# Kernel optimization log

Measured on AMD Instinct MI355X. Metric: run time of the kernel, lower is better.

## Reference

```python
import jax, jax.numpy as jnp
import numpy as np

DIM = 128
HOP = 2
NEIGH = [12, 2]  # neighbor_num per hop
ALPHA = 0.2      # leaky-relu slope
NUM_NODE = 50000
B, S = 128, 50
STDV = 1.0 / np.sqrt(DIM)


def _leaky(x):
    return jnp.where(x >= 0, x, ALPHA * x)


def _local_agg(h, adj, a_local):
    # h: [B,S,D], adj: [B,S,S] ints in 0..4, a_local: [4,D]
    a_in = h[:, :, None, :] * h[:, None, :, :]            # [B,S,S,D]
    e = _leaky(jnp.einsum('bijd,kd->kbij', a_in, a_local))  # [4,B,S,S]
    att = jnp.full(adj.shape, -9e15, dtype=h.dtype)
    for k in range(4):
        att = jnp.where(adj == k + 1, e[k], att)
    att = jax.nn.softmax(att, axis=-1)
    return jnp.einsum('bij,bjd->bid', att, h)


def _global_agg(self_v, neigh_v, extra_v, w1, w2, w3, bias):
    # self_v: [B,N,D], neigh_v: [B,N,K,D], extra_v: [B,N,D]
    a = _leaky(jnp.einsum('bnkd,de->bnke', extra_v[:, :, None, :] * neigh_v, w1))
    a = jnp.einsum('bnke,e->bnk', a, w2)
    a = jax.nn.softmax(a, axis=-1)
    agg = jnp.einsum('bnk,bnkd->bnd', a, neigh_v)
    out = jnp.concatenate([self_v, agg], axis=-1) @ w3 + bias
    return jax.nn.relu(out)


def setup_inputs() -> dict:
    key = jax.random.key(0)
    ks = jax.random.split(key, 12)
    u = lambda k, shp: jax.random.uniform(k, shp, jnp.float32, -STDV, STDV)
    return {
        'inputs': jax.random.randint(ks[0], (B, S), 0, NUM_NODE),
        'adj': jax.random.randint(ks[1], (B, S, S), 0, 5),
        'mask_item': jnp.ones((B, S), dtype=jnp.int32),
        'item': jax.random.randint(ks[2], (B, S), 0, NUM_NODE),
        'first_adj': jax.random.randint(ks[3], (B, S * NEIGH[0]), 0, NUM_NODE),
        'adj_all': jax.random.randint(ks[4], (NUM_NODE, 2), 0, NUM_NODE),
        'embedding': u(ks[5], (NUM_NODE, DIM)),
        'a_local': u(ks[6], (4, DIM)),
        'gw1': u(ks[7], (HOP, DIM, DIM)),
        'gw2': u(ks[8], (HOP, DIM)),
        'gw3': u(ks[9], (HOP, 2 * DIM, DIM)),
        'gbias': u(ks[10], (HOP, DIM)),
    }


def reference(inputs, adj, mask_item, item, first_adj, adj_all,
              embedding, a_local, gw1, gw2, gw3, gbias):
    b, s = inputs.shape
    h = embedding[inputs]                                  # [B,S,D]
    h_local = _local_agg(h, adj, a_local)

    m = mask_item.astype(embedding.dtype)[..., None]       # [B,S,1]
    item_emb = embedding[item] * m
    sum_item = jnp.sum(item_emb, 1) / jnp.sum(m, 1)        # [B,D]
    sess = sum_item[:, None, :]                            # [B,1,D]

    # multi-hop neighbor sampling
    neigh1 = first_adj.reshape(b, s * NEIGH[0])            # [B, 600]
    neigh2 = adj_all[neigh1.reshape(-1)].reshape(b, s * NEIGH[0] * NEIGH[1])  # [B,1200]
    ev = [embedding[inputs], embedding[neigh1], embedding[neigh2]]

    for n_hop in range(HOP):
        nxt = []
        for hop in range(HOP - n_hop):
            neigh_v = ev[hop + 1].reshape(b, -1, NEIGH[hop], DIM)
            extra_v = jnp.broadcast_to(sess, (b, ev[hop].shape[1], DIM))
            nxt.append(_global_agg(ev[hop], neigh_v, extra_v,
                                   gw1[n_hop], gw2[n_hop], gw3[n_hop], gbias[n_hop]))
        ev = nxt
    h_global = ev[0].reshape(b, s, DIM)

    # dropout is identity at eval
    return h_local + h_global
```

## Files before the change

### kernel.cpp

```cpp
#include <hip/hip_runtime.h>
#include <stdint.h>

typedef unsigned short ushort_t;
typedef __attribute__((ext_vector_type(8))) short bf16x8;
typedef __attribute__((ext_vector_type(4))) float f32x4;

#define B_   128
#define S_   50
#define D_   128
#define ALPHA_ 0.2f

__device__ __forceinline__ float bf2f(ushort_t u){
  return __uint_as_float(((uint32_t)u) << 16);
}
__device__ __forceinline__ ushort_t f2bf(float f){
  uint32_t x = __float_as_uint(f);
  x = (x + 0x7fffu + ((x >> 16) & 1u)) >> 16;
  return (ushort_t)x;
}
__device__ __forceinline__ float leaky(float x){ return x >= 0.f ? x : ALPHA_*x; }

__device__ __forceinline__ int detect_flag_block(const uint32_t* __restrict__ emb_raw){
  __shared__ int flg;
  if (threadIdx.x == 0){
    int ok = 1;
    for (int i = 0; i < 64; i++){
      uint32_t lo = emb_raw[i] & 0xffffu;
      uint32_t ex = (lo >> 7) & 0xFFu;
      if (!(lo == 0u || (ex >= 64u && ex <= 126u))) ok = 0;
    }
    flg = ok;
  }
  __syncthreads();
  return flg;
}

#define NLOCAL_ 512
#define NSESS_  64
#define NCVT_   6347
#define NPREP_  48

__global__ __launch_bounds__(256) void k1(
    const int* __restrict__ inputs, const int* __restrict__ adj,
    const int* __restrict__ item, const int* __restrict__ mask,
    const void* __restrict__ p0, const void* __restrict__ p1,
    const void* __restrict__ p2, const void* __restrict__ p3,
    const void* __restrict__ p4, const void* __restrict__ p5,
    ushort_t* __restrict__ emb_b, uint4* __restrict__ w1f, uint4* __restrict__ w3f,
    ushort_t* __restrict__ sessb, ushort_t* __restrict__ hlb)
{
  int blk = blockIdx.x, tid = threadIdx.x;
  int flag = detect_flag_block((const uint32_t*)p0);

  if (blk < NLOCAL_){
    __shared__ ushort_t hS[64][136];
    __shared__ float    attS[16][68];
    __shared__ int      sids[64];
    __shared__ ushort_t alS[512];
    int b  = blk >> 2;
    int mi = blk & 3;
    if (tid < 64) sids[tid] = (tid < S_) ? inputs[b*S_ + tid] : 0;
    for (int i = tid; i < 512; i += 256)
      alS[i] = flag ? ((const ushort_t*)p1)[i] : f2bf(((const float*)p1)[i]);
    __syncthreads();
    if (flag){
      const ushort_t* e16 = (const ushort_t*)p0;
      for (int idx = tid; idx < 64*16; idx += 256){
        int j = idx >> 4, ch = idx & 15;
        uint4 v = {0u, 0u, 0u, 0u};
        if (j < S_) v = *(const uint4*)(e16 + (size_t)sids[j]*D_ + ch*8);
        *(uint4*)(&hS[j][ch*8]) = v;
      }
    } else {
      const float* ef = (const float*)p0;
      for (int idx = tid; idx < 64*32; idx += 256){
        int j = idx >> 5, ch = idx & 31;
        union { ushort_t u[4]; uint2 d2; } o;
        o.d2 = make_uint2(0u, 0u);
        if (j < S_){
          float4 v = *(const float4*)(ef + (size_t)sids[j]*D_ + ch*4);
          o.u[0]=f2bf(v.x); o.u[1]=f2bf(v.y); o.u[2]=f2bf(v.z); o.u[3]=f2bf(v.w);
        }
        *(uint2*)(&hS[j][ch*4]) = o.d2;
      }
    }
    for (int idx = tid; idx < 16*64; idx += 256)
      attS[idx >> 6][idx & 63] = -9.0e15f;
    __syncthreads();

    int lane = tid & 63, wv = tid >> 6;
    int q = lane >> 4, c = lane & 15;

    f32x4 Eacc[4];
    #pragma unroll
    for (int ni = 0; ni < 4; ni++) Eacc[ni] = (f32x4){0.f,0.f,0.f,0.f};
    #pragma unroll
    for (int kt = 0; kt < 4; kt++){
      uint4 av = *(const uint4*)(alS + wv*D_ + kt*32 + q*8);
      const uint32_t* ap = (const uint32_t*)&av;
      uint4 hv = *(const uint4*)(&hS[mi*16 + c][kt*32 + q*8]);
      const uint32_t* hp = (const uint32_t*)&hv;
      union { ushort_t u[8]; bf16x8 v; } afr;
      #pragma unroll
      for (int p = 0; p < 4; p++){
        float x0 = __uint_as_float(hp[p] << 16)         * __uint_as_float(ap[p] << 16);
        float x1 = __uint_as_float(hp[p] & 0xffff0000u) * __uint_as_float(ap[p] & 0xffff0000u);
        afr.u[2*p]   = f2bf(x0);
        afr.u[2*p+1] = f2bf(x1);
      }
      #pragma unroll
      for (int ni = 0; ni < 4; ni++){
        union { uint4 q4; bf16x8 v; } bfr;
        bfr.q4 = *(const uint4*)(&hS[ni*16 + c][kt*32 + q*8]);
        Eacc[ni] = __builtin_amdgcn_mfma_f32_16x16x32_bf16(afr.v, bfr.v, Eacc[ni], 0,0,0);
      }
    }
    const int* adjb = adj + (size_t)b*S_*S_;
    #pragma unroll
    for (int ni = 0; ni < 4; ni++){
      int j = ni*16 + c;
      #pragma unroll
      for (int r = 0; r < 4; r++){
        int i = mi*16 + q*4 + r;
        if (i < S_ && j < S_){
          int kk = adjb[i*S_ + j];
          if (kk == wv + 1) attS[q*4 + r][j] = leaky(Eacc[ni][r]);
        }
      }
    }
    __syncthreads();
    {
      int r  = tid >> 4;
      int cg = tid & 15;
      int i  = mi*16 + r;
      float v0 = attS[r][cg*4+0], v1 = attS[r][cg*4+1];
      float v2 = attS[r][cg*4+2], v3 = attS[r][cg*4+3];
      float mx = fmaxf(fmaxf(v0,v1), fmaxf(v2,v3));
      #pragma unroll
      for (int off = 1; off < 16; off <<= 1) mx = fmaxf(mx, __shfl_xor(mx, off, 16));
      float e0 = (cg*4+0 < S_) ? __expf(v0 - mx) : 0.f;
      float e1 = (cg*4+1 < S_) ? __expf(v1 - mx) : 0.f;
      float e2 = (cg*4+2 < S_) ? __expf(v2 - mx) : 0.f;
      float e3 = (cg*4+3 < S_) ? __expf(v3 - mx) : 0.f;
      float s = e0 + e1 + e2 + e3;
      #pragma unroll
      for (int off = 1; off < 16; off <<= 1) s += __shfl_xor(s, off, 16);
      float inv = (i < S_) ? 1.f / s : 0.f;
      attS[r][cg*4+0] = e0*inv;
      attS[r][cg*4+1] = e1*inv;
      attS[r][cg*4+2] = e2*inv;
      attS[r][cg*4+3] = e3*inv;
    }
    __syncthreads();
    f32x4 Pacc[2];
    Pacc[0] = (f32x4){0.f,0.f,0.f,0.f};
    Pacc[1] = (f32x4){0.f,0.f,0.f,0.f};
    #pragma unroll
    for (int kt = 0; kt < 2; kt++){
      union { ushort_t u[8]; bf16x8 v; } afr;
      const float* arow = &attS[c][kt*32 + q*8];
      #pragma unroll
      for (int j = 0; j < 8; j++) afr.u[j] = f2bf(arow[j]);
      #pragma unroll
      for (int nn = 0; nn < 2; nn++){
        int ni = 2*wv + nn;
        union { ushort_t u[8]; bf16x8 v; } bfr;
        #pragma unroll
        for (int jj = 0; jj < 8; jj++)
          bfr.u[jj] = hS[kt*32 + q*8 + jj][ni*16 + c];
        Pacc[nn] = __builtin_amdgcn_mfma_f32_16x16x32_bf16(afr.v, bfr.v, Pacc[nn], 0,0,0);
      }
    }
    #pragma unroll
    for (int nn = 0; nn < 2; nn++){
      int d = (2*wv + nn)*16 + c;
      #pragma unroll
      for (int r = 0; r < 4; r++){
        int i = mi*16 + q*4 + r;
        if (i < S_) hlb[((size_t)b*S_ + i)*D_ + d] = f2bf(Pacc[nn][r]);
      }
    }
  } else if (blk < NLOCAL_ + NSESS_){
    int b = (blk - NLOCAL_)*2 + (tid >> 7);
    int d = tid & 127;
    float acc = 0.f, den = 0.f;
    if (flag){
      const ushort_t* e16 = (const ushort_t*)p0;
      for (int s = 0; s < S_; s++){
        float fm = (float)mask[b*S_ + s];
        int id = item[b*S_ + s];
        acc += fm * bf2f(e16[(size_t)id*D_ + d]);
        den += fm;
      }
    } else {
      const float* ef = (const float*)p0;
      for (int s = 0; s < S_; s++){
        float fm = (float)mask[b*S_ + s];
        int id = item[b*S_ + s];
        acc += fm * ef[(size_t)id*D_ + d];
        den += fm;
      }
    }
    sessb[b*D_ + d] = f2bf(acc / den);
  } else if (blk < NLOCAL_ + NSESS_ + NCVT_){
    const int seg_end[6] = {6400000, 6400512, 6433280, 6433536, 6499072, 6499328};
    int base = ((blk - NLOCAL_ - NSESS_)*256 + tid) * 4;
    if (base >= 6499328) return;
    int s = 0;
    while (base >= seg_end[s]) s++;
    int segbase = (s == 0) ? 0 : seg_end[s-1];
    const void* src = (s==0)?p0:(s==1)?p1:(s==2)?p2:(s==3)?p3:(s==4)?p4:p5;
    int off = base - segbase;
    union { ushort_t u[4]; uint2 d2; } o;
    if (flag){
      o.d2 = *(const uint2*)((const ushort_t*)src + off);
    } else {
      float4 v = *(const float4*)((const float*)src + off);
      o.u[0] = f2bf(v.x); o.u[1] = f2bf(v.y); o.u[2] = f2bf(v.z); o.u[3] = f2bf(v.w);
    }
    *(uint2*)(emb_b + base) = o.d2;
  } else {
    int id = (blk - NLOCAL_ - NSESS_ - NCVT_)*256 + tid;
    if (id >= 12288) return;
    if (id < 4096){
      int h = id >> 11, i = id & 2047;
      int kt = i >> 9, rem = i & 511, t = rem >> 6, ln = rem & 63;
      int q = ln >> 4, c = ln & 15;
      union { ushort_t u[8]; uint4 q4; } e;
      #pragma unroll
      for (int j = 0; j < 8; j++){
        int idx = h*16384 + (32*kt + q*8 + j)*128 + 16*t + c;
        e.u[j] = flag ? ((const ushort_t*)p2)[idx] : f2bf(((const float*)p2)[idx]);
      }
      w1f[h*2048 + i] = e.q4;
    } else {
      int id2 = id - 4096;
      int h = id2 >> 12, i = id2 & 4095;
      int kt = i >> 9, rem = i & 511, t = rem >> 6, ln = rem & 63;
      int q = ln >> 4, c = ln & 15;
      union { ushort_t u[8]; uint4 q4; } e;
      #pragma unroll
      for (int j = 0; j < 8; j++){
        int idx = h*32768 + (32*kt + q*8 + j)*128 + 16*t + c;
        e.u[j] = flag ? ((const ushort_t*)p4)[idx] : f2bf(((const float*)p4)[idx]);
      }
      w3f[h*4096 + i] = e.q4;
    }
  }
}

__global__ __launch_bounds__(512) void tprep(
    const ushort_t* __restrict__ emb, const uint4* __restrict__ w3f,
    ushort_t* __restrict__ Tt, ushort_t* __restrict__ Tb)
{
  __shared__ uint4 frag[4096];
  int tid = threadIdx.x;
  for (int i = tid; i < 4096; i += 512) frag[i] = w3f[i];
  __syncthreads();
  int lane = tid & 63, wave = tid >> 6;
  int m = lane & 15, q = lane >> 4;
  int row = blockIdx.x*128 + wave*16 + m;
  int rowc = row < 50000 ? row : 49999;
  f32x4 acct[8], accb[8];
  #pragma unroll
  for (int t = 0; t < 8; t++){ acct[t] = (f32x4){0.f,0.f,0.f,0.f}; accb[t] = (f32x4){0.f,0.f,0.f,0.f}; }
  #pragma unroll
  for (int kt = 0; kt < 4; kt++){
    union { uint4 q4; bf16x8 v; } bfr;
    bfr.q4 = *(const uint4*)(emb + (size_t)rowc*D_ + kt*32 + q*8);
    #pragma unroll
    for (int t = 0; t < 8; t++){
      union { uint4 q4; bf16x8 v; } af, af2;
      af.q4  = frag[(kt*8 + t)*64 + lane];
      af2.q4 = frag[((kt+4)*8 + t)*64 + lane];
      acct[t] = __builtin_amdgcn_mfma_f32_16x16x32_bf16(af.v,  bfr.v, acct[t], 0, 0, 0);
      accb[t] = __builtin_amdgcn_mfma_f32_16x16x32_bf16(af2.v, bfr.v, accb[t], 0, 0, 0);
    }
  }
  if (row < 50000){
    #pragma unroll
    for (int t = 0; t < 8; t++){
      int col0 = 16*t + q*4;
      union { ushort_t u[4]; uint2 d2; } pk;
      #pragma unroll
      for (int r = 0; r < 4; r++) pk.u[r] = f2bf(acct[t][r]);
      *(uint2*)(Tt + (size_t)row*D_ + col0) = pk.d2;
      #pragma unroll
      for (int r = 0; r < 4; r++) pk.u[r] = f2bf(accb[t][r]);
      *(uint2*)(Tb + (size_t)row*D_ + col0) = pk.d2;
    }
  }
}

__global__ __launch_bounds__(256) void score_mfma_ab(
    const ushort_t* __restrict__ sessb, const ushort_t* __restrict__ emb,
    const int* __restrict__ neigh1, const int* __restrict__ adj_all,
    const uint4* __restrict__ w1f, const ushort_t* __restrict__ w2,
    float* __restrict__ score, int nA){
  __shared__ uint4 bfrag[2048];
  int tid = threadIdx.x;
  for (int i = tid; i < 2048; i += 256) bfrag[i] = w1f[i];
  __syncthreads();
  int lane = tid & 63, wave = tid >> 6;
  int m = lane & 15, q = lane >> 4;
  float w2v[8];
  #pragma unroll
  for (int t = 0; t < 8; t++) w2v[t] = bf2f(w2[16*t + m]);

  for (int it = 0; it < 2; it++){
    int row_base = blockIdx.x*128 + it*64 + wave*16;
    int row = row_base + m;
    const ushort_t* nrow; int b;
    if (row < nA){
      nrow = emb + (size_t)neigh1[row]*D_;
      b = row / 600;
    } else {
      int r2 = row - nA;
      nrow = emb + (size_t)adj_all[(size_t)neigh1[r2>>1]*2 + (r2&1)]*D_;
      b = r2 / 1200;
    }
    const ushort_t* srow = sessb + (size_t)b*D_;

    f32x4 acc[8];
    #pragma unroll
    for (int t = 0; t < 8; t++) acc[t] = (f32x4){0.f,0.f,0.f,0.f};
    #pragma unroll
    for (int kt = 0; kt < 4; kt++){
      uint4 nv = *(const uint4*)(nrow + kt*32 + q*8);
      uint4 sv = *(const uint4*)(srow + kt*32 + q*8);
      const uint32_t* np = (const uint32_t*)&nv;
      const uint32_t* sp = (const uint32_t*)&sv;
      union { ushort_t u[8]; bf16x8 v; } afr;
      #pragma unroll
      for (int p = 0; p < 4; p++){
        uint32_t n2 = np[p], s2 = sp[p];
        float a0 = __uint_as_float(n2 << 16)          * __uint_as_float(s2 << 16);
        float a1 = __uint_as_float(n2 & 0xffff0000u)  * __uint_as_float(s2 & 0xffff0000u);
        afr.u[2*p]   = f2bf(a0);
        afr.u[2*p+1] = f2bf(a1);
      }
      #pragma unroll
      for (int t = 0; t < 8; t++){
        union { uint4 q4; bf16x8 v; } bfr;
        bfr.q4 = bfrag[(kt*8 + t)*64 + lane];
        acc[t] = __builtin_amdgcn_mfma_f32_16x16x32_bf16(afr.v, bfr.v, acc[t], 0, 0, 0);
      }
    }
    #pragma unroll
    for (int r = 0; r < 4; r++){
      float s = 0.f;
      #pragma unroll
      for (int t = 0; t < 8; t++) s += leaky(acc[t][r]) * w2v[t];
      s += __shfl_xor(s, 1, 64);
      s += __shfl_xor(s, 2, 64);
      s += __shfl_xor(s, 4, 64);
      s += __shfl_xor(s, 8, 64);
      if (m == 0) score[row_base + q*4 + r] = s;
    }
  }
}

__global__ __launch_bounds__(256) void score_mfma_c(
    const ushort_t* __restrict__ sessb, const ushort_t* __restrict__ out1,
    const uint4* __restrict__ w1f, const ushort_t* __restrict__ w2,
    float* __restrict__ score){
  __shared__ uint4 bfrag[2048];
  int tid = threadIdx.x;
  for (int i = tid; i < 2048; i += 256) bfrag[i] = w1f[i];
  __syncthreads();
  int lane = tid & 63, wave = tid >> 6;
  int m = lane & 15, q = lane >> 4;
  float w2v[8];
  #pragma unroll
  for (int t = 0; t < 8; t++) w2v[t] = bf2f(w2[16*t + m]);
  for (int it = 0; it < 2; it++){
    int row_base = blockIdx.x*128 + it*64 + wave*16;
    int row = row_base + m;
    const ushort_t* nrow = out1 + (size_t)row*D_;
    int b = row / 600;
    const ushort_t* srow = sessb + (size_t)b*D_;
    f32x4 acc[8];
    #pragma unroll
    for (int t = 0; t < 8; t++) acc[t] = (f32x4){0.f,0.f,0.f,0.f};
    #pragma unroll
    for (int kt = 0; kt < 4; kt++){
      uint4 nv = *(const uint4*)(nrow + kt*32 + q*8);
      uint4 sv = *(const uint4*)(srow + kt*32 + q*8);
      const uint32_t* np = (const uint32_t*)&nv;
      const uint32_t* sp = (const uint32_t*)&sv;
      union { ushort_t u[8]; bf16x8 v; } afr;
      #pragma unroll
      for (int p = 0; p < 4; p++){
        uint32_t n2 = np[p], s2 = sp[p];
        float a0 = __uint_as_float(n2 << 16)          * __uint_as_float(s2 << 16);
        float a1 = __uint_as_float(n2 & 0xffff0000u)  * __uint_as_float(s2 & 0xffff0000u);
        afr.u[2*p]   = f2bf(a0);
        afr.u[2*p+1] = f2bf(a1);
      }
      #pragma unroll
      for (int t = 0; t < 8; t++){
        union { uint4 q4; bf16x8 v; } bfr;
        bfr.q4 = bfrag[(kt*8 + t)*64 + lane];
        acc[t] = __builtin_amdgcn_mfma_f32_16x16x32_bf16(afr.v, bfr.v, acc[t], 0, 0, 0);
      }
    }
    #pragma unroll
    for (int r = 0; r < 4; r++){
      float s = 0.f;
      #pragma unroll
      for (int t = 0; t < 8; t++) s += leaky(acc[t][r]) * w2v[t];
      s += __shfl_xor(s, 1, 64);
      s += __shfl_xor(s, 2, 64);
      s += __shfl_xor(s, 4, 64);
      s += __shfl_xor(s, 8, 64);
      if (m == 0) score[row_base + q*4 + r] = s;
    }
  }
}

template<int K>
__device__ __forceinline__ void softmaxK(const float* __restrict__ sc, float att[K]){
  float mx = -__builtin_inff();
  #pragma unroll
  for (int k = 0; k < K; k++){ att[k] = sc[k]; mx = fmaxf(mx, att[k]); }
  float s = 0.f;
  #pragma unroll
  for (int k = 0; k < K; k++){ att[k] = __expf(att[k] - mx); s += att[k]; }
  float inv = 1.f / s;
  #pragma unroll
  for (int k = 0; k < K; k++) att[k] *= inv;
}

template<int K>
__device__ __forceinline__ void out_tile(
    int lane, const uint4* __restrict__ afrag,
    const ushort_t* __restrict__ sptr, const ushort_t* const nptr[K],
    const float att[K], f32x4 acc[8]){
  int q = lane >> 4;
  #pragma unroll
  for (int kt = 0; kt < 8; kt++){
    union { ushort_t u[8]; uint4 q4; bf16x8 v; } bfr;
    if (kt < 4){
      bfr.q4 = *(const uint4*)(sptr + kt*32 + q*8);
    } else {
      float g[8] = {0,0,0,0,0,0,0,0};
      #pragma unroll
      for (int k = 0; k < K; k++){
        uint4 nv = *(const uint4*)(nptr[k] + (kt-4)*32 + q*8);
        const uint32_t* np = (const uint32_t*)&nv;
        #pragma unroll
        for (int p = 0; p < 4; p++){
          g[2*p]   = fmaf(att[k], __uint_as_float(np[p] << 16),         g[2*p]);
          g[2*p+1] = fmaf(att[k], __uint_as_float(np[p] & 0xffff0000u), g[2*p+1]);
        }
      }
      #pragma unroll
      for (int j = 0; j < 8; j++) bfr.u[j] = f2bf(g[j]);
    }
    #pragma unroll
    for (int t = 0; t < 8; t++){
      union { uint4 q4; bf16x8 v; } af;
      af.q4 = afrag[(kt*8 + t)*64 + lane];
      acc[t] = __builtin_amdgcn_mfma_f32_16x16x32_bf16(af.v, bfr.v, acc[t], 0, 0, 0);
    }
  }
}

__global__ __launch_bounds__(256) void gather_out(
    const int* __restrict__ idx, const int* __restrict__ nbr,
    const int* __restrict__ adj_all, const float* __restrict__ score,
    const ushort_t* __restrict__ Tt, const ushort_t* __restrict__ Tb,
    const ushort_t* __restrict__ bias,
    ushort_t* __restrict__ o0c, ushort_t* __restrict__ out1c,
    int nA50, int nTot, int scoreBbase)
{
  int row  = (blockIdx.x*256 + threadIdx.x) >> 6;
  int lane = threadIdx.x & 63;
  if (row >= nTot) return;
  row = __builtin_amdgcn_readfirstlane(row);
  float b0 = bf2f(bias[lane*2]), b1 = bf2f(bias[lane*2 + 1]);
  float acc0, acc1;
  ushort_t* dst;
  if (row < nA50){
    float att[12];
    softmaxK<12>(score + (size_t)row*12, att);
    uint32_t sv = *(const uint32_t*)(Tt + (size_t)idx[row]*D_ + lane*2);
    acc0 = __uint_as_float(sv << 16);
    acc1 = __uint_as_float(sv & 0xffff0000u);
    #pragma unroll
    for (int k = 0; k < 12; k++){
      uint32_t nv = *(const uint32_t*)(Tb + (size_t)nbr[row*12 + k]*D_ + lane*2);
      acc0 = fmaf(att[k], __uint_as_float(nv << 16),          acc0);
      acc1 = fmaf(att[k], __uint_as_float(nv & 0xffff0000u),  acc1);
    }
    dst = o0c + (size_t)row*D_;
  } else {
    int rB = row - nA50;
    float att[2];
    softmaxK<2>(score + scoreBbase + (size_t)rB*2, att);
    int self = nbr[rB];
    uint32_t sv = *(const uint32_t*)(Tt + (size_t)self*D_ + lane*2);
    acc0 = __uint_as_float(sv << 16);
    acc1 = __uint_as_float(sv & 0xffff0000u);
    #pragma unroll
    for (int k = 0; k < 2; k++){
      uint32_t nv = *(const uint32_t*)(Tb + (size_t)adj_all[(size_t)self*2 + k]*D_ + lane*2);
      acc0 = fmaf(att[k], __uint_as_float(nv << 16),          acc0);
      acc1 = fmaf(att[k], __uint_as_float(nv & 0xffff0000u),  acc1);
    }
    dst = out1c + (size_t)rB*D_;
  }
  union { ushort_t u[2]; uint32_t d; } pk;
  pk.u[0] = f2bf(fmaxf(acc0 + b0, 0.f));
  pk.u[1] = f2bf(fmaxf(acc1 + b1, 0.f));
  *(uint32_t*)(dst + lane*2) = pk.d;
}

__global__ __launch_bounds__(512) void out_mfma_ab(
    const float* __restrict__ score, const int* __restrict__ idx,
    const int* __restrict__ nbr, const int* __restrict__ adj_all,
    const ushort_t* __restrict__ emb, const uint4* __restrict__ w3f,
    const ushort_t* __restrict__ bias,
    ushort_t* __restrict__ o0c, ushort_t* __restrict__ out1c,
    int nA, int nTot, int scoreBbase){
  __shared__ uint4 afrag[4096];
  int tid = threadIdx.x;
  for (int i = tid; i < 4096; i += 512) afrag[i] = w3f[i];
  __syncthreads();
  int lane = tid & 63, wave = tid >> 6;
  int mrow = lane & 15, q = lane >> 4;
  float bv[8][4];
  #pragma unroll
  for (int t = 0; t < 8; t++){
    const ushort_t* bp = bias + 16*t + q*4;
    #pragma unroll
    for (int r = 0; r < 4; r++) bv[t][r] = bf2f(bp[r]);
  }
  int row_base = blockIdx.x*128 + wave*16;
  int row = row_base + mrow;
  bool active = row < nTot;
  int rowc = active ? row : (nTot - 1);
  bool isA = rowc < nA;
  f32x4 acc[8];
  #pragma unroll
  for (int t = 0; t < 8; t++) acc[t] = (f32x4){0.f,0.f,0.f,0.f};
  if (isA){
    const ushort_t* sptr = emb + (size_t)idx[rowc]*D_;
    const ushort_t* nptr[12];
    #pragma unroll
    for (int k = 0; k < 12; k++) nptr[k] = emb + (size_t)nbr[rowc*12 + k]*D_;
    float att[12];
    softmaxK<12>(score + (size_t)rowc*12, att);
    out_tile<12>(lane, afrag, sptr, nptr, att, acc);
  } else {
    int rB = rowc - nA;
    const ushort_t* sptr = emb + (size_t)nbr[rB]*D_;
    const ushort_t* nptr[2];
    #pragma unroll
    for (int k = 0; k < 2; k++) nptr[k] = emb + (size_t)adj_all[(size_t)nbr[rB]*2 + k]*D_;
    float att[2];
    softmaxK<2>(score + scoreBbase + (size_t)rB*2, att);
    out_tile<2>(lane, afrag, sptr, nptr, att, acc);
  }
  if (active){
    ushort_t* dst = isA ? (o0c + (size_t)row*D_) : (out1c + (size_t)(row - nA)*D_);
    #pragma unroll
    for (int t = 0; t < 8; t++){
      int col0 = 16*t + q*4;
      union { ushort_t u[4]; uint2 d2; } pk;
      #pragma unroll
// ... 26 lines not shown
  bool active = row < nrows;
  int rowc = active ? row : (nrows - 1);
  const ushort_t* sptr = selfsrc + (size_t)rowc*D_;
  const ushort_t* nptr[12];
  #pragma unroll
  for (int k = 0; k < 12; k++) nptr[k] = out1 + (size_t)(rowc*12 + k)*D_;
  float att[12];
  softmaxK<12>(score + (size_t)rowc*12, att);
  f32x4 acc[8];
  #pragma unroll
  for (int t = 0; t < 8; t++) acc[t] = (f32x4){0.f,0.f,0.f,0.f};
  out_tile<12>(lane, afrag, sptr, nptr, att, acc);
  if (active){
    #pragma unroll
    for (int t = 0; t < 8; t++){
      int col0 = 16*t + q*4;
      float v[4];
      const ushort_t* ap = addsrc + (size_t)row*D_ + col0;
      #pragma unroll
      for (int r = 0; r < 4; r++)
        v[r] = fmaxf(acc[t][r] + bv[t][r], 0.f) + bf2f(ap[r]);
      *(f32x4*)(outf + (size_t)row*D_ + col0) = (f32x4){v[0], v[1], v[2], v[3]};
    }
  }
}

extern "C" void kernel_launch(void* const* d_in, const int* in_sizes, int n_in,
                              void* d_out, int out_size, void* d_ws, size_t ws_size,
                              hipStream_t stream) {
  const int* inputs    = (const int*)d_in[0];
  const int* adj       = (const int*)d_in[1];
  const int* mask_item = (const int*)d_in[2];
  const int* item      = (const int*)d_in[3];
  const int* first_adj = (const int*)d_in[4];
  const int* adj_all   = (const int*)d_in[5];

  char* ws = (char*)d_ws;
  size_t o = 0;
  ushort_t* emb_b  = (ushort_t*)(ws + o); o += 12800000;
  ushort_t* alocb  = (ushort_t*)(ws + o); o += 1024;
  ushort_t* gw1b   = (ushort_t*)(ws + o); o += 65536;
  ushort_t* gw2b   = (ushort_t*)(ws + o); o += 512;
  ushort_t* gw3b   = (ushort_t*)(ws + o); o += 131072;
  ushort_t* gbb    = (ushort_t*)(ws + o); o += 512;
  ushort_t* sessb  = (ushort_t*)(ws + o); o += 32768;
  ushort_t* hlb    = (ushort_t*)(ws + o); o += 1638400;
  uint4*    w1f    = (uint4*)(ws + o);    o += 65536;
  uint4*    w3f    = (uint4*)(ws + o);    o += 131072;
  size_t fixed = o;
  (void)alocb; (void)gw1b; (void)gw3b;

  float* outp = (float*)d_out;

  k1<<<NLOCAL_ + NSESS_ + NCVT_ + NPREP_, 256, 0, stream>>>(
      inputs, adj, item, mask_item,
      d_in[6], d_in[7], d_in[8], d_in[9], d_in[10], d_in[11],
      emb_b, w1f, w3f, sessb, hlb);

  const size_t TPATH_NEED = fixed + 2*(size_t)12800000
                          + (size_t)128*153600
                          + (size_t)128*12800
                          + (size_t)3*128*600*4;
  if (ws_size >= TPATH_NEED){
    ushort_t* Tt    = (ushort_t*)(ws + o);  o += 12800000;
    ushort_t* Tb    = (ushort_t*)(ws + o);  o += 12800000;
    ushort_t* out1c = (ushort_t*)(ws + o);  o += (size_t)128*153600;
    ushort_t* o0c   = (ushort_t*)(ws + o);  o += (size_t)128*12800;
    float*    score = (float*)(ws + o);
    int nA600 = 128*600, nA50 = 128*50, nTot = 128*650;

    tprep<<<391, 512, 0, stream>>>(emb_b, w3f, Tt, Tb);
    score_mfma_ab<<<(3*nA600)/128, 256, 0, stream>>>(sessb, emb_b, first_adj, adj_all,
                                                     w1f, gw2b, score, nA600);
    gather_out<<<(nTot*64 + 255)/256, 256, 0, stream>>>(inputs, first_adj, adj_all, score,
                                                        Tt, Tb, gbb, o0c, out1c,
                                                        nA50, nTot, nA600);
    score_mfma_c<<<nA600/128, 256, 0, stream>>>(sessb, out1c, w1f + 2048, gw2b + 128, score);
    out_mfma_c<<<(nA50 + 127)/128, 512, 0, stream>>>(score, out1c, o0c,
                                                     w3f + 4096, gbb + 128,
                                                     hlb, outp, nA50);
  } else {
    int CHB = 16;
    if      (ws_size >= fixed + (size_t)128*173600) CHB = 128;
    else if (ws_size >= fixed + (size_t)64 *173600) CHB = 64;
    else if (ws_size >= fixed + (size_t)32 *173600) CHB = 32;
    ushort_t* out1c = (ushort_t*)(ws + o);  o += (size_t)CHB*153600;
    ushort_t* o0c   = (ushort_t*)(ws + o);  o += (size_t)CHB*12800;
    float*    score = (float*)(ws + o);

    int nchunk = B_ / CHB;
    for (int c = 0; c < nchunk; c++){
      int b0 = c * CHB;
      const int* fadj  = first_adj + (size_t)b0 * 600;
      const ushort_t* sbc = sessb + (size_t)b0 * D_;
      ushort_t*  hlc   = hlb  + (size_t)b0 * 50 * D_;
      float*     outc  = outp + (size_t)b0 * 50 * D_;
      int nA600 = CHB*600, nA50 = CHB*50, nTot = CHB*650;

      score_mfma_ab<<<(3*nA600)/128, 256, 0, stream>>>(sbc, emb_b, fadj, adj_all,
                                                       w1f, gw2b, score, nA600);
      out_mfma_ab<<<(nTot + 127)/128, 512, 0, stream>>>(score, inputs + b0*50, fadj, adj_all,
                                                        emb_b, w3f, gbb, o0c, out1c,
                                                        nA50, nTot, nA600);
      score_mfma_c<<<nA600/128, 256, 0, stream>>>(sbc, out1c, w1f + 2048, gw2b + 128, score);
      out_mfma_c<<<(nA50 + 127)/128, 512, 0, stream>>>(score, out1c, o0c,
                                                       w3f + 4096, gbb + 128,
                                                       hlc, outc, nA50);
    }
  }
}
```

Measured before the change: 194.0 us.

## Fuse transform precompute into k1 and fold session vector into per-batch W1

Moves the embedding-times-W3 precompute (Tt/Tb) from its own kernel into extra blocks of the first fused kernel, converting directly from the raw input embeddings. The score kernels are restructured per batch: the session vector is multiplied into the W1 fragments once per block, so neighbor rows feed the MFMA directly with no elementwise product. Grid shapes change to per-batch row groups, and the final output kernel uses smaller 64-row blocks for more parallelism. The cost is W1 fragments rebuilt per block and more shared-memory sharing inside k1, which could lower occupancy for the local-attention blocks.

```diff
diff --git a/kernel.cpp b/kernel.cpp
--- a/kernel.cpp
+++ b/kernel.cpp
@@ -37,8 +37,13 @@
 
 #define NLOCAL_ 512
 #define NSESS_  64
+#define NTPREP_ 1564
 #define NCVT_   6347
 #define NPREP_  48
+#define TPREP_BASE_ (NLOCAL_ + NSESS_)
+#define CVT_BASE_   (TPREP_BASE_ + NTPREP_)
+#define PREP_BASE_  (CVT_BASE_ + NCVT_)
+#define K1_GRID_    (PREP_BASE_ + NPREP_)
 
 __global__ __launch_bounds__(256) void k1(
     const int* __restrict__ inputs, const int* __restrict__ adj,
@@ -47,29 +52,31 @@
     const void* __restrict__ p2, const void* __restrict__ p3,
     const void* __restrict__ p4, const void* __restrict__ p5,
     ushort_t* __restrict__ emb_b, uint4* __restrict__ w1f, uint4* __restrict__ w3f,
-    ushort_t* __restrict__ sessb, ushort_t* __restrict__ hlb)
+    ushort_t* __restrict__ sessb, ushort_t* __restrict__ hlb,
+    ushort_t* __restrict__ Tt, ushort_t* __restrict__ Tb)
 {
+  __shared__ uint4 smem[2048];
   int blk = blockIdx.x, tid = threadIdx.x;
   int flag = detect_flag_block((const uint32_t*)p0);
 
   if (blk < NLOCAL_){
-    __shared__ ushort_t hS[64][136];
-    __shared__ float    attS[16][68];
-    __shared__ int      sids[64];
-    __shared__ ushort_t alS[512];
+    ushort_t* hSp   = (ushort_t*)smem;
+    float*    attSp = (float*)((char*)smem + 17408);
+    int*      sidsp = (int*)((char*)smem + 21760);
+    ushort_t* alSp  = (ushort_t*)((char*)smem + 22016);
     int b  = blk >> 2;
     int mi = blk & 3;
-    if (tid < 64) sids[tid] = (tid < S_) ? inputs[b*S_ + tid] : 0;
+    if (tid < 64) sidsp[tid] = (tid < S_) ? inputs[b*S_ + tid] : 0;
     for (int i = tid; i < 512; i += 256)
-      alS[i] = flag ? ((const ushort_t*)p1)[i] : f2bf(((const float*)p1)[i]);
+      alSp[i] = flag ? ((const ushort_t*)p1)[i] : f2bf(((const float*)p1)[i]);
     __syncthreads();
     if (flag){
       const ushort_t* e16 = (const ushort_t*)p0;
       for (int idx = tid; idx < 64*16; idx += 256){
         int j = idx >> 4, ch = idx & 15;
         uint4 v = {0u, 0u, 0u, 0u};
-        if (j < S_) v = *(const uint4*)(e16 + (size_t)sids[j]*D_ + ch*8);
-        *(uint4*)(&hS[j][ch*8]) = v;
+        if (j < S_) v = *(const uint4*)(e16 + (size_t)sidsp[j]*D_ + ch*8);
+        *(uint4*)(hSp + j*136 + ch*8) = v;
       }
     } else {
       const float* ef = (const float*)p0;
@@ -78,14 +85,14 @@
         union { ushort_t u[4]; uint2 d2; } o;
         o.d2 = make_uint2(0u, 0u);
         if (j < S_){
-          float4 v = *(const float4*)(ef + (size_t)sids[j]*D_ + ch*4);
+          float4 v = *(const float4*)(ef + (size_t)sidsp[j]*D_ + ch*4);
           o.u[0]=f2bf(v.x); o.u[1]=f2bf(v.y); o.u[2]=f2bf(v.z); o.u[3]=f2bf(v.w);
         }
-        *(uint2*)(&hS[j][ch*4]) = o.d2;
+        *(uint2*)(hSp + j*136 + ch*4) = o.d2;
       }
     }
     for (int idx = tid; idx < 16*64; idx += 256)
-      attS[idx >> 6][idx & 63] = -9.0e15f;
+      attSp[(idx >> 6)*68 + (idx & 63)] = -9.0e15f;
     __syncthreads();
 
     int lane = tid & 63, wv = tid >> 6;
@@ -96,9 +103,9 @@
     for (int ni = 0; ni < 4; ni++) Eacc[ni] = (f32x4){0.f,0.f,0.f,0.f};
     #pragma unroll
     for (int kt = 0; kt < 4; kt++){
-      uint4 av = *(const uint4*)(alS + wv*D_ + kt*32 + q*8);
+      uint4 av = *(const uint4*)(alSp + wv*D_ + kt*32 + q*8);
       const uint32_t* ap = (const uint32_t*)&av;
-      uint4 hv = *(const uint4*)(&hS[mi*16 + c][kt*32 + q*8]);
+      uint4 hv = *(const uint4*)(hSp + (mi*16 + c)*136 + kt*32 + q*8);
       const uint32_t* hp = (const uint32_t*)&hv;
       union { ushort_t u[8]; bf16x8 v; } afr;
       #pragma unroll
@@ -111,7 +118,7 @@
       #pragma unroll
       for (int ni = 0; ni < 4; ni++){
         union { uint4 q4; bf16x8 v; } bfr;
-        bfr.q4 = *(const uint4*)(&hS[ni*16 + c][kt*32 + q*8]);
+        bfr.q4 = *(const uint4*)(hSp + (ni*16 + c)*136 + kt*32 + q*8);
         Eacc[ni] = __builtin_amdgcn_mfma_f32_16x16x32_bf16(afr.v, bfr.v, Eacc[ni], 0,0,0);
       }
     }
@@ -124,7 +131,7 @@
         int i = mi*16 + q*4 + r;
         if (i < S_ && j < S_){
           int kk = adjb[i*S_ + j];
-          if (kk == wv + 1) attS[q*4 + r][j] = leaky(Eacc[ni][r]);
+          if (kk == wv + 1) attSp[(q*4 + r)*68 + j] = leaky(Eacc[ni][r]);
         }
       }
     }
@@ -133,8 +140,8 @@
       int r  = tid >> 4;
       int cg = tid & 15;
       int i  = mi*16 + r;
-      float v0 = attS[r][cg*4+0], v1 = attS[r][cg*4+1];
-      float v2 = attS[r][cg*4+2], v3 = attS[r][cg*4+3];
+      float v0 = attSp[r*68 + cg*4+0], v1 = attSp[r*68 + cg*4+1];
+      float v2 = attSp[r*68 + cg*4+2], v3 = attSp[r*68 + cg*4+3];
       float mx = fmaxf(fmaxf(v0,v1), fmaxf(v2,v3));
       #pragma unroll
       for (int off = 1; off < 16; off <<= 1) mx = fmaxf(mx, __shfl_xor(mx, off, 16));
@@ -146,10 +153,10 @@
       #pragma unroll
       for (int off = 1; off < 16; off <<= 1) s += __shfl_xor(s, off, 16);
       float inv = (i < S_) ? 1.f / s : 0.f;
-      attS[r][cg*4+0] = e0*inv;
-      attS[r][cg*4+1] = e1*inv;
-      attS[r][cg*4+2] = e2*inv;
-      attS[r][cg*4+3] = e3*inv;
+      attSp[r*68 + cg*4+0] = e0*inv;
+      attSp[r*68 + cg*4+1] = e1*inv;
+      attSp[r*68 + cg*4+2] = e2*inv;
+      attSp[r*68 + cg*4+3] = e3*inv;
     }
     __syncthreads();
     f32x4 Pacc[2];
@@ -158,7 +165,7 @@
     #pragma unroll
     for (int kt = 0; kt < 2; kt++){
       union { ushort_t u[8]; bf16x8 v; } afr;
-      const float* arow = &attS[c][kt*32 + q*8];
+      const float* arow = attSp + c*68 + kt*32 + q*8;
       #pragma unroll
       for (int j = 0; j < 8; j++) afr.u[j] = f2bf(arow[j]);
       #pragma unroll
@@ -167,7 +174,7 @@
         union { ushort_t u[8]; bf16x8 v; } bfr;
         #pragma unroll
         for (int jj = 0; jj < 8; jj++)
-          bfr.u[jj] = hS[kt*32 + q*8 + jj][ni*16 + c];
+          bfr.u[jj] = hSp[(kt*32 + q*8 + jj)*136 + ni*16 + c];
         Pacc[nn] = __builtin_amdgcn_mfma_f32_16x16x32_bf16(afr.v, bfr.v, Pacc[nn], 0,0,0);
       }
     }
@@ -202,9 +209,63 @@
       }
     }
     sessb[b*D_ + d] = f2bf(acc / den);
-  } else if (blk < NLOCAL_ + NSESS_ + NCVT_){
+  } else if (blk < CVT_BASE_){
+    if (!Tt) return;
+    int tp   = blk - TPREP_BASE_;
+    int half = tp & 1;
+    int rowbase = (tp >> 1) * 64;
+    for (int i = tid; i < 2048; i += 256){
+      int kt = i >> 9, rem = i & 511, t = rem >> 6, ln = rem & 63;
+      int q = ln >> 4, c = ln & 15;
+      union { ushort_t u[8]; uint4 q4; } e;
+      #pragma unroll
+      for (int j = 0; j < 8; j++){
+        int idx = (32*(half*4 + kt) + q*8 + j)*128 + 16*t + c;
+        e.u[j] = flag ? ((const ushort_t*)p4)[idx] : f2bf(((const float*)p4)[idx]);
+      }
+      smem[i] = e.q4;
+    }
+    __syncthreads();
+    int lane = tid & 63, wave = tid >> 6;
+    int m = lane & 15, q = lane >> 4;
+    int row = rowbase + wave*16 + m;
+    int rowc = row < 50000 ? row : 49999;
+    f32x4 acc[8];
+    #pragma unroll
+    for (int t = 0; t < 8; t++) acc[t] = (f32x4){0.f,0.f,0.f,0.f};
+    #pragma unroll
+    for (int kt = 0; kt < 4; kt++){
+      union { ushort_t u[8]; uint4 q4; bf16x8 v; } bfr;
+      if (flag){
+        bfr.q4 = *(const uint4*)((const ushort_t*)p0 + (size_t)rowc*D_ + kt*32 + q*8);
+      } else {
+        const float* ef = (const float*)p0 + (size_t)rowc*D_ + kt*32 + q*8;
+        float4 f0 = *(const float4*)(ef);
+        float4 f1 = *(const float4*)(ef + 4);
+        bfr.u[0]=f2bf(f0.x); bfr.u[1]=f2bf(f0.y); bfr.u[2]=f2bf(f0.z); bfr.u[3]=f2bf(f0.w);
+        bfr.u[4]=f2bf(f1.x); bfr.u[5]=f2bf(f1.y); bfr.u[6]=f2bf(f1.z); bfr.u[7]=f2bf(f1.w);
+      }
+      #pragma unroll
+      for (int t = 0; t < 8; t++){
+        union { uint4 q4; bf16x8 v; } af;
+        af.q4 = smem[(kt*8 + t)*64 + lane];
+        acc[t] = __builtin_amdgcn_mfma_f32_16x16x32_bf16(af.v, bfr.v, acc[t], 0, 0, 0);
+      }
+    }
+    if (row < 50000){
+      ushort_t* dst = (half ? Tb : Tt) + (size_t)row*D_;
+      #pragma unroll
+      for (int t = 0; t < 8; t++){
+        int col0 = 16*t + q*4;
+        union { ushort_t u[4]; uint2 d2; } pk;
+        #pragma unroll
+        for (int r = 0; r < 4; r++) pk.u[r] = f2bf(acc[t][r]);
+        *(uint2*)(dst + col0) = pk.d2;
+      }
+    }
+  } else if (blk < PREP_BASE_){
     const int seg_end[6] = {6400000, 6400512, 6433280, 6433536, 6499072, 6499328};
-    int base = ((blk - NLOCAL_ - NSESS_)*256 + tid) * 4;
+    int base = ((blk - CVT_BASE_)*256 + tid) * 4;
     if (base >= 6499328) return;
     int s = 0;
     while (base >= seg_end[s]) s++;
@@ -220,7 +281,7 @@
     }
     *(uint2*)(emb_b + base) = o.d2;
   } else {
-    int id = (blk - NLOCAL_ - NSESS_ - NCVT_)*256 + tid;
+    int id = (blk - PREP_BASE_)*256 + tid;
     if (id >= 12288) return;
     if (id < 4096){
       int h = id >> 11, i = id & 2047;
@@ -249,57 +310,32 @@
   }
 }
 
-__global__ __launch_bounds__(512) void tprep(
-    const ushort_t* __restrict__ emb, const uint4* __restrict__ w3f,
-    ushort_t* __restrict__ Tt, ushort_t* __restrict__ Tb)
-{
-  __shared__ uint4 frag[4096];
-  int tid = threadIdx.x;
-  for (int i = tid; i < 4096; i += 512) frag[i] = w3f[i];
-  __syncthreads();
-  int lane = tid & 63, wave = tid >> 6;
-  int m = lane & 15, q = lane >> 4;
-  int row = blockIdx.x*128 + wave*16 + m;
-  int rowc = row < 50000 ? row : 49999;
-  f32x4 acct[8], accb[8];
-  #pragma unroll
-  for (int t = 0; t < 8; t++){ acct[t] = (f32x4){0.f,0.f,0.f,0.f}; accb[t] = (f32x4){0.f,0.f,0.f,0.f}; }
-  #pragma unroll
-  for (int kt = 0; kt < 4; kt++){
-    union { uint4 q4; bf16x8 v; } bfr;
-    bfr.q4 = *(const uint4*)(emb + (size_t)rowc*D_ + kt*32 + q*8);
-    #pragma unroll
-    for (int t = 0; t < 8; t++){
-      union { uint4 q4; bf16x8 v; } af, af2;
-      af.q4  = frag[(kt*8 + t)*64 + lane];
-      af2.q4 = frag[((kt+4)*8 + t)*64 + lane];
-      acct[t] = __builtin_amdgcn_mfma_f32_16x16x32_bf16(af.v,  bfr.v, acct[t], 0, 0, 0);
-      accb[t] = __builtin_amdgcn_mfma_f32_16x16x32_bf16(af2.v, bfr.v, accb[t], 0, 0, 0);
-    }
-  }
-  if (row < 50000){
-    #pragma unroll
-    for (int t = 0; t < 8; t++){
-      int col0 = 16*t + q*4;
-      union { ushort_t u[4]; uint2 d2; } pk;
-      #pragma unroll
-      for (int r = 0; r < 4; r++) pk.u[r] = f2bf(acct[t][r]);
-      *(uint2*)(Tt + (size_t)row*D_ + col0) = pk.d2;
-      #pragma unroll
-      for (int r = 0; r < 4; r++) pk.u[r] = f2bf(accb[t][r]);
-      *(uint2*)(Tb + (size_t)row*D_ + col0) = pk.d2;
-    }
-  }
-}
-
-__global__ __launch_bounds__(256) void score_mfma_ab(
+__global__ __launch_bounds__(256) void score2_ab(
     const ushort_t* __restrict__ sessb, const ushort_t* __restrict__ emb,
     const int* __restrict__ neigh1, const int* __restrict__ adj_all,
     const uint4* __restrict__ w1f, const ushort_t* __restrict__ w2,
-    float* __restrict__ score, int nA){
+    float* __restrict__ score)
+{
   __shared__ uint4 bfrag[2048];
-  int tid = threadIdx.x;
-  for (int i = tid; i < 2048; i += 256) bfrag[i] = w1f[i];
+  __shared__ ushort_t sS[128];
+  int blk = blockIdx.x, tid = threadIdx.x;
+  int sb  = blk / 6;
+  int sub = blk - sb*6;
+  int grp = sub >> 1;
+  int halft = sub & 1;
+  if (tid < 16) ((uint4*)sS)[tid] = ((const uint4*)(sessb + (size_t)sb*D_))[tid];
+  __syncthreads();
+  for (int i = tid; i < 2048; i += 256){
+    int kt = i >> 9, ln = i & 63, q = (ln >> 4);
+    uint4 w = w1f[i];
+    uint4 sv = *(const uint4*)(sS + kt*32 + q*8);
+    const ushort_t* wu = (const ushort_t*)&w;
+    const ushort_t* su = (const ushort_t*)&sv;
+    union { ushort_t u[8]; uint4 q4; } o;
+    #pragma unroll
+    for (int j = 0; j < 8; j++) o.u[j] = f2bf(bf2f(wu[j]) * bf2f(su[j]));
+    bfrag[i] = o.q4;
+  }
   __syncthreads();
   int lane = tid & 63, wave = tid >> 6;
   int m = lane & 15, q = lane >> 4;
@@ -307,113 +343,115 @@
   #pragma unroll
   for (int t = 0; t < 8; t++) w2v[t] = bf2f(w2[16*t + m]);
 
-  for (int it = 0; it < 2; it++){
-    int row_base = blockIdx.x*128 + it*64 + wave*16;
-    int row = row_base + m;
-    const ushort_t* nrow; int b;
-    if (row < nA){
-      nrow = emb + (size_t)neigh1[row]*D_;
-      b = row / 600;
+  int tend = halft ? 38 : 19;
+  for (int t = halft*19 + wave; t < tend; t += 4){
+    int rr = t*16 + m;
+    int rrc = rr < 599 ? rr : 599;
+    int nid;
+    if (grp == 0){
+      nid = neigh1[sb*600 + rrc];
     } else {
-      int r2 = row - nA;
-      nrow = emb + (size_t)adj_all[(size_t)neigh1[r2>>1]*2 + (r2&1)]*D_;
-      b = r2 / 1200;
-    }
-    const ushort_t* srow = sessb + (size_t)b*D_;
-
+      int r2 = sb*1200 + (grp-1)*600 + rrc;
+      nid = adj_all[(size_t)neigh1[r2 >> 1]*2 + (r2 & 1)];
+    }
+    const ushort_t* nrow = emb + (size_t)nid*D_;
     f32x4 acc[8];
     #pragma unroll
-    for (int t = 0; t < 8; t++) acc[t] = (f32x4){0.f,0.f,0.f,0.f};
+    for (int t8 = 0; t8 < 8; t8++) acc[t8] = (f32x4){0.f,0.f,0.f,0.f};
     #pragma unroll
     for (int kt = 0; kt < 4; kt++){
-      uint4 nv = *(const uint4*)(nrow + kt*32 + q*8);
-      uint4 sv = *(const uint4*)(srow + kt*32 + q*8);
-      const uint32_t* np = (const uint32_t*)&nv;
-      const uint32_t* sp = (const uint32_t*)&sv;
-      union { ushort_t u[8]; bf16x8 v; } afr;
-      #pragma unroll
-      for (int p = 0; p < 4; p++){
-        uint32_t n2 = np[p], s2 = sp[p];
-        float a0 = __uint_as_float(n2 << 16)          * __uint_as_float(s2 << 16);
-        float a1 = __uint_as_float(n2 & 0xffff0000u)  * __uint_as_float(s2 & 0xffff0000u);
-        afr.u[2*p]   = f2bf(a0);
-        afr.u[2*p+1] = f2bf(a1);
-      }
-      #pragma unroll
-      for (int t = 0; t < 8; t++){
-        union { uint4 q4; bf16x8 v; } bfr;
-        bfr.q4 = bfrag[(kt*8 + t)*64 + lane];
-        acc[t] = __builtin_amdgcn_mfma_f32_16x16x32_bf16(afr.v, bfr.v, acc[t], 0, 0, 0);
+      union { uint4 q4; bf16x8 v; } af;
+      af.q4 = *(const uint4*)(nrow + kt*32 + q*8);
+      #pragma unroll
+      for (int t8 = 0; t8 < 8; t8++){
+        union { uint4 q4; bf16x8 v; } bf;
+        bf.q4 = bfrag[(kt*8 + t8)*64 + lane];
+        acc[t8] = __builtin_amdgcn_mfma_f32_16x16x32_bf16(af.v, bf.v, acc[t8], 0, 0, 0);
       }
     }
     #pragma unroll
     for (int r = 0; r < 4; r++){
       float s = 0.f;
       #pragma unroll
-      for (int t = 0; t < 8; t++) s += leaky(acc[t][r]) * w2v[t];
+      for (int t8 = 0; t8 < 8; t8++) s += leaky(acc[t8][r]) * w2v[t8];
       s += __shfl_xor(s, 1, 64);
       s += __shfl_xor(s, 2, 64);
       s += __shfl_xor(s, 4, 64);
       s += __shfl_xor(s, 8, 64);
-      if (m == 0) score[row_base + q*4 + r] = s;
-    }
-  }
-}
-
-__global__ __launch_bounds__(256) void score_mfma_c(
+      if (m == 0){
+        int rw = t*16 + q*4 + r;
+        if (rw < 600){
+          int sidx = (grp == 0) ? (sb*600 + rw)
+                                : (76800 + sb*1200 + (grp-1)*600 + rw);
+          score[sidx] = s;
+        }
+      }
+    }
+  }
+}
+
+__global__ __launch_bounds__(256) void score2_c(
     const ushort_t* __restrict__ sessb, const ushort_t* __restrict__ out1,
     const uint4* __restrict__ w1f, const ushort_t* __restrict__ w2,
-    float* __restrict__ score){
+    float* __restrict__ score)
+{
   __shared__ uint4 bfrag[2048];
-  int tid = threadIdx.x;
-  for (int i = tid; i < 2048; i += 256) bfrag[i] = w1f[i];
+  __shared__ ushort_t sS[128];
+  int blk = blockIdx.x, tid = threadIdx.x;
+  int sb  = blk >> 2;
+  int qtr = blk & 3;
+  if (tid < 16) ((uint4*)sS)[tid] = ((const uint4*)(sessb + (size_t)sb*D_))[tid];
+  __syncthreads();
+  for (int i = tid; i < 2048; i += 256){
+    int kt = i >> 9, ln = i & 63, q = (ln >> 4);
+    uint4 w = w1f[i];
+    uint4 sv = *(const uint4*)(sS + kt*32 + q*8);
+    const ushort_t* wu = (const ushort_t*)&w;
+    const ushort_t* su = (const ushort_t*)&sv;
+    union { ushort_t u[8]; uint4 q4; } o;
+    #pragma unroll
+    for (int j = 0; j < 8; j++) o.u[j] = f2bf(bf2f(wu[j]) * bf2f(su[j]));
+    bfrag[i] = o.q4;
+  }
   __syncthreads();
   int lane = tid & 63, wave = tid >> 6;
   int m = lane & 15, q = lane >> 4;
   float w2v[8];
   #pragma unroll
   for (int t = 0; t < 8; t++) w2v[t] = bf2f(w2[16*t + m]);
-  for (int it = 0; it < 2; it++){
-    int row_base = blockIdx.x*128 + it*64 + wave*16;
-    int row = row_base + m;
-    const ushort_t* nrow = out1 + (size_t)row*D_;
-    int b = row / 600;
-    const ushort_t* srow = sessb + (size_t)b*D_;
+
+  int t0 = qtr*10, tend = (qtr*10 + 10 < 38) ? qtr*10 + 10 : 38;
+  for (int t = t0 + wave; t < tend; t += 4){
+    int rr = t*16 + m;
+    int rrc = rr < 599 ? rr : 599;
+    const ushort_t* nrow = out1 + ((size_t)sb*600 + rrc)*D_;
     f32x4 acc[8];
     #pragma unroll
-    for (int t = 0; t < 8; t++) acc[t] = (f32x4){0.f,0.f,0.f,0.f};
+    for (int t8 = 0; t8 < 8; t8++) acc[t8] = (f32x4){0.f,0.f,0.f,0.f};
     #pragma unroll
     for (int kt = 0; kt < 4; kt++){
-      uint4 nv = *(const uint4*)(nrow + kt*32 + q*8);
-      uint4 sv = *(const uint4*)(srow + kt*32 + q*8);
-      const uint32_t* np = (const uint32_t*)&nv;
-      const uint32_t* sp = (const uint32_t*)&sv;
-      union { ushort_t u[8]; bf16x8 v; } afr;
-      #pragma unroll
-      for (int p = 0; p < 4; p++){
-        uint32_t n2 = np[p], s2 = sp[p];
-        float a0 = __uint_as_float(n2 << 16)          * __uint_as_float(s2 << 16);
-        float a1 = __uint_as_float(n2 & 0xffff0000u)  * __uint_as_float(s2 & 0xffff0000u);
-        afr.u[2*p]   = f2bf(a0);
-        afr.u[2*p+1] = f2bf(a1);
-      }
-      #pragma unroll
-      for (int t = 0; t < 8; t++){
-        union { uint4 q4; bf16x8 v; } bfr;
-        bfr.q4 = bfrag[(kt*8 + t)*64 + lane];
-        acc[t] = __builtin_amdgcn_mfma_f32_16x16x32_bf16(afr.v, bfr.v, acc[t], 0, 0, 0);
+      union { uint4 q4; bf16x8 v; } af;
+      af.q4 = *(const uint4*)(nrow + kt*32 + q*8);
+      #pragma unroll
+      for (int t8 = 0; t8 < 8; t8++){
+        union { uint4 q4; bf16x8 v; } bf;
+        bf.q4 = bfrag[(kt*8 + t8)*64 + lane];
+        acc[t8] = __builtin_amdgcn_mfma_f32_16x16x32_bf16(af.v, bf.v, acc[t8], 0, 0, 0);
       }
     }
     #pragma unroll
     for (int r = 0; r < 4; r++){
       float s = 0.f;
       #pragma unroll
-      for (int t = 0; t < 8; t++) s += leaky(acc[t][r]) * w2v[t];
+      for (int t8 = 0; t8 < 8; t8++) s += leaky(acc[t8][r]) * w2v[t8];
       s += __shfl_xor(s, 1, 64);
       s += __shfl_xor(s, 2, 64);
       s += __shfl_xor(s, 4, 64);
       s += __shfl_xor(s, 8, 64);
-      if (m == 0) score[row_base + q*4 + r] = s;
+      if (m == 0){
+        int rw = t*16 + q*4 + r;
+        if (rw < 600) score[sb*600 + rw] = s;
+      }
     }
   }
 }
@@ -516,6 +554,178 @@
   *(uint32_t*)(dst + lane*2) = pk.d;
 }
 
+__global__ __launch_bounds__(256) void out_mfma_c2(
+    const float* __restrict__ score, const ushort_t* __restrict__ out1,
+    const ushort_t* __restrict__ selfsrc, const uint4* __restrict__ w3f,
+    const ushort_t* __restrict__ bias,
+    const ushort_t* __restrict__ addsrc, float* __restrict__ outf, int nrows){
+  __shared__ uint4 afrag[4096];
+  int tid = threadIdx.x;
+  for (int i = tid; i < 4096; i += 256) afrag[i] = w3f[i];
+  __syncthreads();
+  int lane = tid & 63, wave = tid >> 6;
+  int mrow = lane & 15, q = lane >> 4;
+  float bv[8][4];
+  #pragma unroll
+  for (int t = 0; t < 8; t++){
+    const ushort_t* bp = bias + 16*t + q*4;
+    #pragma unroll
+    for (int r = 0; r < 4; r++) bv[t][r] = bf2f(bp[r]);
+  }
+  int row_base = blockIdx.x*64 + wave*16;
+  int row = row_base + mrow;
+  bool active = row < nrows;
+  int rowc = active ? row : (nrows - 1);
+  const ushort_t* sptr = selfsrc + (size_t)rowc*D_;
+  const ushort_t* nptr[12];
+  #pragma unroll
+  for (int k = 0; k < 12; k++) nptr[k] = out1 + (size_t)(rowc*12 + k)*D_;
+  float att[12];
+  softmaxK<12>(score + (size_t)rowc*12, att);
+  f32x4 acc[8];
+  #pragma unroll
+  for (int t = 0; t < 8; t++) acc[t] = (f32x4){0.f,0.f,0.f,0.f};
+  out_tile<12>(lane, afrag, sptr, nptr, att, acc);
+  if (active){
+    #pragma unroll
+    for (int t = 0; t < 8; t++){
+      int col0 = 16*t + q*4;
+      float v[4];
+      const ushort_t* ap = addsrc + (size_t)row*D_ + col0;
+      #pragma unroll
+      for (int r = 0; r < 4; r++)
+        v[r] = fmaxf(acc[t][r] + bv[t][r], 0.f) + bf2f(ap[r]);
+      *(f32x4*)(outf + (size_t)row*D_ + col0) = (f32x4){v[0], v[1], v[2], v[3]};
+    }
+  }
+}
+
+__global__ __launch_bounds__(256) void score_mfma_ab(
+    const ushort_t* __restrict__ sessb, const ushort_t* __restrict__ emb,
+    const int* __restrict__ neigh1, const int* __restrict__ adj_all,
+    const uint4* __restrict__ w1f, const ushort_t* __restrict__ w2,
+    float* __restrict__ score, int nA){
+  __shared__ uint4 bfrag[2048];
+  int tid = threadIdx.x;
+  for (int i = tid; i < 2048; i += 256) bfrag[i] = w1f[i];
+  __syncthreads();
+  int lane = tid & 63, wave = tid >> 6;
+  int m = lane & 15, q = lane >> 4;
+  float w2v[8];
+  #pragma unroll
+  for (int t = 0; t < 8; t++) w2v[t] = bf2f(w2[16*t + m]);
+
+  for (int it = 0; it < 2; it++){
+    int row_base = blockIdx.x*128 + it*64 + wave*16;
+    int row = row_base + m;
+    const ushort_t* nrow; int b;
+    if (row < nA){
+      nrow = emb + (size_t)neigh1[row]*D_;
+      b = row / 600;
+    } else {
+      int r2 = row - nA;
+      nrow = emb + (size_t)adj_all[(size_t)neigh1[r2>>1]*2 + (r2&1)]*D_;
+      b = r2 / 1200;
+    }
+    const ushort_t* srow = sessb + (size_t)b*D_;
+
+    f32x4 acc[8];
+    #pragma unroll
+    for (int t = 0; t < 8; t++) acc[t] = (f32x4){0.f,0.f,0.f,0.f};
+    #pragma unroll
+    for (int kt = 0; kt < 4; kt++){
+      uint4 nv = *(const uint4*)(nrow + kt*32 + q*8);
+      uint4 sv = *(const uint4*)(srow + kt*32 + q*8);
+      const uint32_t* np = (const uint32_t*)&nv;
+      const uint32_t* sp = (const uint32_t*)&sv;
+      union { ushort_t u[8]; bf16x8 v; } afr;
+      #pragma unroll
+      for (int p = 0; p < 4; p++){
+        uint32_t n2 = np[p], s2 = sp[p];
+        float a0 = __uint_as_float(n2 << 16)          * __uint_as_float(s2 << 16);
+        float a1 = __uint_as_float(n2 & 0xffff0000u)  * __uint_as_float(s2 & 0xffff0000u);
+        afr.u[2*p]   = f2bf(a0);
+        afr.u[2*p+1] = f2bf(a1);
+      }
+      #pragma unroll
+      for (int t = 0; t < 8; t++){
+        union { uint4 q4; bf16x8 v; } bfr;
+        bfr.q4 = bfrag[(kt*8 + t)*64 + lane];
+        acc[t] = __builtin_amdgcn_mfma_f32_16x16x32_bf16(afr.v, bfr.v, acc[t], 0, 0, 0);
+      }
+    }
+    #pragma unroll
+    for (int r = 0; r < 4; r++){
+      float s = 0.f;
+      #pragma unroll
+      for (int t = 0; t < 8; t++) s += leaky(acc[t][r]) * w2v[t];
+      s += __shfl_xor(s, 1, 64);
+      s += __shfl_xor(s, 2, 64);
+      s += __shfl_xor(s, 4, 64);
+      s += __shfl_xor(s, 8, 64);
+      if (m == 0) score[row_base + q*4 + r] = s;
+    }
+  }
+}
+
+__global__ __launch_bounds__(256) void score_mfma_c(
+    const ushort_t* __restrict__ sessb, const ushort_t* __restrict__ out1,
+    const uint4* __restrict__ w1f, const ushort_t* __restrict__ w2,
+    float* __restrict__ score){
+  __shared__ uint4 bfrag[2048];
+  int tid = threadIdx.x;
+  for (int i = tid; i < 2048; i += 256) bfrag[i] = w1f[i];
+  __syncthreads();
+  int lane = tid & 63, wave = tid >> 6;
+  int m = lane & 15, q = lane >> 4;
+  float w2v[8];
+  #pragma unroll
+  for (int t = 0; t < 8; t++) w2v[t] = bf2f(w2[16*t + m]);
+  for (int it = 0; it < 2; it++){
+    int row_base = blockIdx.x*128 + it*64 + wave*16;
+    int row = row_base + m;
+    const ushort_t* nrow = out1 + (size_t)row*D_;
+    int b = row / 600;
+    const ushort_t* srow = sessb + (size_t)b*D_;
+    f32x4 acc[8];
+    #pragma unroll
+    for (int t = 0; t < 8; t++) acc[t] = (f32x4){0.f,0.f,0.f,0.f};
+    #pragma unroll
+    for (int kt = 0; kt < 4; kt++){
+      uint4 nv = *(const uint4*)(nrow + kt*32 + q*8);
+      uint4 sv = *(const uint4*)(srow + kt*32 + q*8);
+      const uint32_t* np = (const uint32_t*)&nv;
+      const uint32_t* sp = (const uint32_t*)&sv;
+      union { ushort_t u[8]; bf16x8 v; } afr;
+      #pragma unroll
+      for (int p = 0; p < 4; p++){
+        uint32_t n2 = np[p], s2 = sp[p];
+        float a0 = __uint_as_float(n2 << 16)          * __uint_as_float(s2 << 16);
+        float a1 = __uint_as_float(n2 & 0xffff0000u)  * __uint_as_float(s2 & 0xffff0000u);
+        afr.u[2*p]   = f2bf(a0);
+        afr.u[2*p+1] = f2bf(a1);
+      }
+      #pragma unroll
+      for (int t = 0; t < 8; t++){
+        union { uint4 q4; bf16x8 v; } bfr;
+        bfr.q4 = bfrag[(kt*8 + t)*64 + lane];
+        acc[t] = __builtin_amdgcn_mfma_f32_16x16x32_bf16(afr.v, bfr.v, acc[t], 0, 0, 0);
+      }
+    }
+    #pragma unroll
+    for (int r = 0; r < 4; r++){
+      float s = 0.f;
+      #pragma unroll
+      for (int t = 0; t < 8; t++) s += leaky(acc[t][r]) * w2v[t];
+      s += __shfl_xor(s, 1, 64);
+      s += __shfl_xor(s, 2, 64);
+      s += __shfl_xor(s, 4, 64);
+      s += __shfl_xor(s, 8, 64);
+      if (m == 0) score[row_base + q*4 + r] = s;
+    }
+  }
+}
+
 __global__ __launch_bounds__(512) void out_mfma_ab(
     const float* __restrict__ score, const int* __restrict__ idx,
     const int* __restrict__ nbr, const int* __restrict__ adj_all,
@@ -648,33 +858,38 @@
 
   float* outp = (float*)d_out;
 
-  k1<<<NLOCAL_ + NSESS_ + NCVT_ + NPREP_, 256, 0, stream>>>(
-      inputs, adj, item, mask_item,
-      d_in[6], d_in[7], d_in[8], d_in[9], d_in[10], d_in[11],
-      emb_b, w1f, w3f, sessb, hlb);
-
   const size_t TPATH_NEED = fixed + 2*(size_t)12800000
                           + (size_t)128*153600
                           + (size_t)128*12800
                           + (size_t)3*128*600*4;
-  if (ws_size >= TPATH_NEED){
-    ushort_t* Tt    = (ushort_t*)(ws + o);  o += 12800000;
-    ushort_t* Tb    = (ushort_t*)(ws + o);  o += 12800000;
+  bool tpath = (ws_size >= TPATH_NEED);
+
+  ushort_t* Tt = nullptr; ushort_t* Tb = nullptr;
+  if (tpath){
+    Tt = (ushort_t*)(ws + o);  o += 12800000;
+    Tb = (ushort_t*)(ws + o);  o += 12800000;
+  }
+
+  k1<<<K1_GRID_, 256, 0, stream>>>(
+      inputs, adj, item, mask_item,
+      d_in[6], d_in[7], d_in[8], d_in[9], d_in[10], d_in[11],
+      emb_b, w1f, w3f, sessb, hlb, Tt, Tb);
+
+  if (tpath){
     ushort_t* out1c = (ushort_t*)(ws + o);  o += (size_t)128*153600;
     ushort_t* o0c   = (ushort_t*)(ws + o);  o += (size_t)128*12800;
     float*    score = (float*)(ws + o);
     int nA600 = 128*600, nA50 = 128*50, nTot = 128*650;
 
-    tprep<<<391, 512, 0, stream>>>(emb_b, w3f, Tt, Tb);
-    score_mfma_ab<<<(3*nA600)/128, 256, 0, stream>>>(sessb, emb_b, first_adj, adj_all,
-                                                     w1f, gw2b, score, nA600);
+    score2_ab<<<768, 256, 0, stream>>>(sessb, emb_b, first_adj, adj_all,
+                                       w1f, gw2b, score);
     gather_out<<<(nTot*64 + 255)/256, 256, 0, stream>>>(inputs, first_adj, adj_all, score,
                                                         Tt, Tb, gbb, o0c, out1c,
                                                         nA50, nTot, nA600);
-    score_mfma_c<<<nA600/128, 256, 0, stream>>>(sessb, out1c, w1f + 2048, gw2b + 128, score);
-    out_mfma_c<<<(nA50 + 127)/128, 512, 0, stream>>>(score, out1c, o0c,
-                                                     w3f + 4096, gbb + 128,
-                                                     hlb, outp, nA50);
+    score2_c<<<512, 256, 0, stream>>>(sessb, out1c, w1f + 2048, gw2b + 128, score);
+    out_mfma_c2<<<(nA50 + 63)/64, 256, 0, stream>>>(score, out1c, o0c,
+                                                    w3f + 4096, gbb + 128,
+                                                    hlb, outp, nA50);
   } else {
     int CHB = 16;
     if      (ws_size >= fixed + (size_t)128*173600) CHB = 128;
```

After: 222.8 us. 14.9% more time.
